# Performance work log

Hardware: AMD Instinct MI355X
Metric: run time of the kernel (lower is better)

The kernel has to match this reference:

```python
import jax, jax.numpy as jnp
import numpy as np

N, F, E, FE, H, OUT = 20000, 128, 320000, 16, 128, 128
NTYPES = 2  # types = (0, 1)
NPAIRS = NTYPES * NTYPES


def setup_inputs() -> dict:
    key = jax.random.key(0)
    ks = jax.random.split(key, 12)
    edge_in_dim = 2 * F + FE
    node_in_dim = F + H
    s = lambda *shape: 1.0 / np.sqrt(shape[-2])
    return {
        "x": jax.random.normal(ks[0], (N, 1, F), dtype=jnp.float32),
        "edge_index": jax.random.randint(ks[1], (2, E), 0, N, dtype=jnp.int64),
        "edge_attr": jax.random.normal(ks[2], (E, FE), dtype=jnp.float32),
        "node_type": jax.random.randint(ks[3], (N,), 0, NTYPES, dtype=jnp.int64),
        # edge MLP params, stacked over the 4 (t1,t2) type pairs
        "ew1": jax.random.normal(ks[4], (NPAIRS, edge_in_dim, H), dtype=jnp.float32) * (1.0 / np.sqrt(edge_in_dim)),
        "eb1": jnp.zeros((NPAIRS, H), dtype=jnp.float32),
        "ew2": jax.random.normal(ks[5], (NPAIRS, H, H), dtype=jnp.float32) * (1.0 / np.sqrt(H)),
        "eb2": jnp.zeros((NPAIRS, H), dtype=jnp.float32),
        # node MLP params, stacked over the 2 node types
        "nw1": jax.random.normal(ks[6], (NTYPES, node_in_dim, H), dtype=jnp.float32) * (1.0 / np.sqrt(node_in_dim)),
        "nb1": jnp.zeros((NTYPES, H), dtype=jnp.float32),
        "nw2": jax.random.normal(ks[7], (NTYPES, H, OUT), dtype=jnp.float32) * (1.0 / np.sqrt(H)),
        "nb2": jnp.zeros((NTYPES, OUT), dtype=jnp.float32),
    }


def reference(x, edge_index, edge_attr, node_type, ew1, eb1, ew2, eb2, nw1, nb1, nw2, nb2):
    x0 = x[:, 0]  # [N, F]
    row, col = edge_index[0], edge_index[1]

    # ---- edge model: type-pair-dispatched 2-layer ReLU MLP ----
    edge_in = jnp.concatenate([x0[row], x0[col], edge_attr], axis=-1)  # [E, 2F+FE]
    h1 = jax.nn.relu(jnp.einsum("ei,pih->eph", edge_in, ew1) + eb1)    # [E, P, H]
    h2 = jax.nn.relu(jnp.einsum("eph,phk->epk", h1, ew2) + eb2)        # [E, P, H]
    pair_id = node_type[row] * NTYPES + node_type[col]                  # [E]
    pair_oh = jax.nn.one_hot(pair_id, NPAIRS, dtype=h2.dtype)           # [E, P]
    edge_feat = jnp.einsum("epk,ep->ek", h2, pair_oh)                   # [E, H]

    # ---- aggregation: sum over incoming edges per source (row) node ----
    agg = jax.ops.segment_sum(edge_feat, row, num_segments=N)           # [N, H]

    # ---- node model: type-dispatched 2-layer MLP + residual ----
    node_in = jnp.concatenate([x0, agg], axis=-1)                       # [N, F+H]
    n1 = jax.nn.relu(jnp.einsum("ni,tih->nth", node_in, nw1) + nb1)     # [N, T, H]
    n2 = jnp.einsum("nth,thk->ntk", n1, nw2) + nb2                      # [N, T, OUT]
    type_oh = jax.nn.one_hot(node_type, NTYPES, dtype=n2.dtype)         # [N, T]
    out = jnp.einsum("ntk,nt->nk", n2, type_oh)                         # [N, OUT]
    out = out + x0[:, :OUT]  # residual
    return out[:, None, :]  # [N, 1, OUT]
```

## Files before the change

### kernel.cpp

```cpp
#include <hip/hip_runtime.h>

#define N_NODES 20000
#define N_EDGES 320000
#define NBINS   (4*N_NODES)
#define SCAN_NBLK 313
#define PRECONV_NBLK 11216
#define HIST_NBLK 1250

typedef unsigned short u16;
typedef __attribute__((ext_vector_type(8))) short bf16x8;
typedef __attribute__((ext_vector_type(4))) float f32x4;
typedef __attribute__((ext_vector_type(4))) unsigned int u32x4;
typedef __attribute__((ext_vector_type(2))) unsigned int u32x2;

__device__ __forceinline__ float b2f(u16 b){
  unsigned u = ((unsigned)b) << 16; float f; __builtin_memcpy(&f, &u, 4); return f;
}
__device__ __forceinline__ u16 f2b(float f){
  unsigned u; __builtin_memcpy(&u, &f, 4); u += 0x7FFF + ((u >> 16) & 1); return (u16)(u >> 16);
}
__device__ __forceinline__ unsigned cvtpk(float a, float b){
  unsigned r;
  asm("v_cvt_pk_bf16_f32 %0, %1, %2" : "=v"(r) : "v"(a), "v"(b));
  return r;
}

#define NX   (N_NODES*128)
#define NW1T (4*288*128)
#define NW2T (4*128*128)
#define NN1  (2*256*128)
#define NN2  (2*128*128)

__global__ void k_prep(const float* __restrict__ x,
                       const float* __restrict__ ew1, const float* __restrict__ ew2,
                       const float* __restrict__ nw1, const float* __restrict__ nw2,
                       u16* __restrict__ x0b,
                       u16* __restrict__ wt1t, u16* __restrict__ wt2t,
                       u16* __restrict__ nw1t, u16* __restrict__ nw2t,
                       const int* __restrict__ ei, const int* __restrict__ ntp,
                       int* __restrict__ hist, int* __restrict__ hist_nt,
                       u16* __restrict__ srank)
{
  int bid = blockIdx.x;
  if (bid >= PRECONV_NBLK) {
    int t = (bid - PRECONV_NBLK) * 256 + threadIdx.x;
    int lane = threadIdx.x & 63;
    if (t < N_EDGES) {
      int r = ei[t], c = ei[N_EDGES + t];
      int tr = ntp[r], tc = ntp[c];
      int key = (tr * 2 + tc) * N_NODES + r;
      int rk = atomicAdd(&hist[key], 1);
      srank[t] = (u16)rk;
    }
    bool valid = t < N_NODES;
    int ty = valid ? ntp[t] : -1;
    unsigned long long m0 = __ballot(ty == 0);
    unsigned long long m1 = __ballot(ty == 1);
    if (lane == 0) {
      int c0 = __popcll(m0), c1 = __popcll(m1);
      if (c0) atomicAdd(&hist_nt[0], c0);
      if (c1) atomicAdd(&hist_nt[1], c1);
    }
    return;
  }
  int t = bid * 256 + threadIdx.x;
  if (t < NX) { x0b[t] = f2b(x[t]); return; }
  t -= NX;
  if (t < NW1T) {
    int p = t / 36864, r = t % 36864; int k = r >> 7, n = r & 127;
    float v = (k < 272) ? ew1[(p * 272 + k) * 128 + n] : 0.f;
    wt1t[(p * 128 + n) * 288 + k] = f2b(v);
    return;
  }
  t -= NW1T;
  if (t < NW2T) {
    int p = t >> 14, r = t & 16383; int k = r >> 7, n = r & 127;
    wt2t[(p * 128 + n) * 128 + k] = f2b(ew2[(p * 128 + k) * 128 + n]);
    return;
  }
  t -= NW2T;
  if (t < NN1) {
    int ty = t >> 15, r = t & 32767; int k = r >> 7, n = r & 127;
    nw1t[(ty * 128 + n) * 256 + k] = f2b(nw1[(ty * 256 + k) * 128 + n]);
    return;
  }
  t -= NN1;
  if (t < NN2) {
    int ty = t >> 14, r = t & 16383; int k = r >> 7, n = r & 127;
    nw2t[(ty * 128 + n) * 128 + k] = f2b(nw2[(ty * 128 + k) * 128 + n]);
  }
}

__global__ void k_scan1(const int* __restrict__ hist, int* __restrict__ parts)
{
  __shared__ int s[256];
  int i = blockIdx.x * 256 + threadIdx.x;
  s[threadIdx.x] = (i < NBINS) ? hist[i] : 0;
  __syncthreads();
  for (int off = 128; off > 0; off >>= 1) {
    if (threadIdx.x < off) s[threadIdx.x] += s[threadIdx.x + off];
    __syncthreads();
  }
  if (threadIdx.x == 0) parts[blockIdx.x] = s[0];
}

__global__ void k_scan2(int* __restrict__ parts)
{
  __shared__ int s[512];
  int t = threadIdx.x;
  int v = (t < SCAN_NBLK) ? parts[t] : 0;
  s[t] = v; __syncthreads();
  for (int off = 1; off < 512; off <<= 1) {
    int xv = (t >= off) ? s[t - off] : 0;
    __syncthreads();
    s[t] += xv;
    __syncthreads();
  }
  if (t < SCAN_NBLK) parts[t] = s[t] - v;
}

__global__ void k_scan3(const int* __restrict__ hist, const int* __restrict__ parts,
                        int* __restrict__ bstart)
{
  __shared__ int s[256];
  int i = blockIdx.x * 256 + threadIdx.x;
  int v = (i < NBINS) ? hist[i] : 0;
  s[threadIdx.x] = v; __syncthreads();
  for (int off = 1; off < 256; off <<= 1) {
    int xv = (threadIdx.x >= off) ? s[threadIdx.x - off] : 0;
    __syncthreads();
    s[threadIdx.x] += xv;
    __syncthreads();
  }
  int excl = s[threadIdx.x] - v + parts[blockIdx.x];
  if (i < NBINS) bstart[i] = excl;
  if (i == 0) bstart[NBINS] = N_EDGES;
}

__global__ void k_place(const int* __restrict__ ei, const int* __restrict__ ntp,
                        const u16* __restrict__ srank, const int* __restrict__ bstart,
                        int2* __restrict__ sedge,
                        int* __restrict__ cur_nt, const int* __restrict__ hist_nt,
                        int* __restrict__ nidx)
{
  int t = blockIdx.x * 256 + threadIdx.x;
  int lane = threadIdx.x & 63;
  if (t < N_EDGES) {
    int r = ei[t], c = ei[N_EDGES + t];
    int tr = ntp[r], tc = ntp[c];
    int key = (tr * 2 + tc) * N_NODES + r;
    int pos = bstart[key] + (int)srank[t];
    int2 v; v.x = r | (c << 15); v.y = t;
    sedge[pos] = v;
  }
  bool valid = t < N_NODES;
  int ty = valid ? ntp[t] : -1;
  unsigned long long m0 = __ballot(ty == 0);
  unsigned long long m1 = __ballot(ty == 1);
  int b0 = 0, b1 = 0;
  if (lane == 0) {
    int c0 = __popcll(m0), c1 = __popcll(m1);
    if (c0) b0 = atomicAdd(&cur_nt[0], c0);
    if (c1) b1 = atomicAdd(&cur_nt[1], c1);
  }
  b0 = __shfl(b0, 0); b1 = __shfl(b1, 0);
  if (valid) {
    unsigned long long lt = (1ull << lane) - 1ull;
    int pos = (ty == 0) ? (b0 + __popcll(m0 & lt))
                        : (hist_nt[0] + b1 + __popcll(m1 & lt));
    nidx[pos] = t;
  }
}

__launch_bounds__(1024, 4)
__global__ void k_edge(const u16* __restrict__ x0b, const float* __restrict__ ea,
                       const u16* __restrict__ wt1t, const u16* __restrict__ wt2t,
                       const float* __restrict__ eb1, const float* __restrict__ eb2,
                       const int* __restrict__ bstart, const int2* __restrict__ sedge,
                       u16* __restrict__ h2s)
{
  __shared__ u16 sW1[128 * 296];
  __shared__ u16 sW2[128 * 136];
  __shared__ u16 slab[16][16][80];
  __shared__ float sEb1[128];
  __shared__ float sEb2[128];

  const int p    = blockIdx.y;
  const int tid  = threadIdx.x;
  const int lane = tid & 63;
  const int wv   = tid >> 6;
  const int llo  = lane & 15;
  const int lhi  = lane >> 4;

  const int base_p = bstart[p * N_NODES];
  const int end_p  = bstart[(p + 1) * N_NODES];

  for (int i = tid; i < 128 * 36; i += 1024) {
    int n = i / 36, c = i % 36;
    *(u32x4*)&sW1[n * 296 + c * 8] = *(const u32x4*)&wt1t[(p * 128 + n) * 288 + c * 8];
  }
  for (int i = tid; i < 128 * 16; i += 1024) {
    int n = i >> 4, c = i & 15;
    *(u32x4*)&sW2[n * 136 + c * 8] = *(const u32x4*)&wt2t[(p * 128 + n) * 128 + c * 8];
  }
  if (tid < 128) sEb1[tid] = eb1[p * 128 + tid];
  else if (tid < 256) sEb2[tid - 128] = eb2[p * 128 + tid - 128];
  __syncthreads();

  for (int g = blockIdx.x * 16 + wv; ; g += gridDim.x * 16) {
    const int es = base_p + g * 32;
    if (es >= end_p) break;

    int pos[2], row[2], col[2], eid[2];
    #pragma unroll
    for (int j = 0; j < 2; ++j) {
      pos[j] = es + j * 16 + llo;
      int pc = pos[j] < end_p ? pos[j] : end_p - 1;
      int2 m = sedge[pc];
      row[j] = m.x & 32767; col[j] = m.x >> 15; eid[j] = m.y;
    }

    bf16x8 xr[2][4], xc[2][4], eaf[2];
    #pragma unroll
    for (int j = 0; j < 2; ++j) {
      #pragma unroll
      for (int ck = 0; ck < 4; ++ck) {
        xr[j][ck] = *(const bf16x8*)&x0b[row[j] * 128 + ck * 32 + lhi * 8];
        xc[j][ck] = *(const bf16x8*)&x0b[col[j] * 128 + ck * 32 + lhi * 8];
      }
      u32x4 pk = (u32x4){0u, 0u, 0u, 0u};
      if (lhi < 2) {
        f32x4 f0 = *(const f32x4*)&ea[eid[j] * 16 + lhi * 8];
        f32x4 f1 = *(const f32x4*)&ea[eid[j] * 16 + lhi * 8 + 4];
        pk[0] = cvtpk(f0[0], f0[1]); pk[1] = cvtpk(f0[2], f0[3]);
        pk[2] = cvtpk(f1[0], f1[1]); pk[3] = cvtpk(f1[2], f1[3]);
      }
      __builtin_memcpy(&eaf[j], &pk, 16);
    }

    f32x4 acc[8][2];
    #pragma unroll
    for (int i = 0; i < 8; ++i) {
      acc[i][0] = (f32x4){0.f, 0.f, 0.f, 0.f};
      acc[i][1] = (f32x4){0.f, 0.f, 0.f, 0.f};
    }

    #pragma unroll
    for (int ck = 0; ck < 4; ++ck) {
      #pragma unroll
      for (int i = 0; i < 8; ++i) {
        bf16x8 wa = *(const bf16x8*)&sW1[(i * 16 + llo) * 296 + ck * 32 + lhi * 8];
        acc[i][0] = __builtin_amdgcn_mfma_f32_16x16x32_bf16(wa, xr[0][ck], acc[i][0], 0, 0, 0);
        acc[i][1] = __builtin_amdgcn_mfma_f32_16x16x32_bf16(wa, xr[1][ck], acc[i][1], 0, 0, 0);
      }
    }
    #pragma unroll
    for (int ck = 0; ck < 4; ++ck) {
      #pragma unroll
      for (int i = 0; i < 8; ++i) {
        bf16x8 wb = *(const bf16x8*)&sW1[(i * 16 + llo) * 296 + 128 + ck * 32 + lhi * 8];
        acc[i][0] = __builtin_amdgcn_mfma_f32_16x16x32_bf16(wb, xc[0][ck], acc[i][0], 0, 0, 0);
        acc[i][1] = __builtin_amdgcn_mfma_f32_16x16x32_bf16(wb, xc[1][ck], acc[i][1], 0, 0, 0);
      }
    }
    #pragma unroll
    for (int i = 0; i < 8; ++i) {
      bf16x8 wce = *(const bf16x8*)&sW1[(i * 16 + llo) * 296 + 256 + lhi * 8];
      acc[i][0] = __builtin_amdgcn_mfma_f32_16x16x32_bf16(wce, eaf[0], acc[i][0], 0, 0, 0);
      acc[i][1] = __builtin_amdgcn_mfma_f32_16x16x32_bf16(wce, eaf[1], acc[i][1], 0, 0, 0);
    }

    bf16x8 h1f[2][4];
    #pragma unroll
    for (int j = 0; j < 2; ++j) {
      #pragma unroll
      for (int ph = 0; ph < 2; ++ph) {
        #pragma unroll
        for (int ii = 0; ii < 4; ++ii) {
          const int i = ph * 4 + ii;
          const f32x4 bb = *(const f32x4*)&sEb1[i * 16 + lhi * 4];
          float v0 = acc[i][j][0] + bb[0]; v0 = v0 > 0.f ? v0 : 0.f;
          float v1 = acc[i][j][1] + bb[1]; v1 = v1 > 0.f ? v1 : 0.f;
          float v2 = acc[i][j][2] + bb[2]; v2 = v2 > 0.f ? v2 : 0.f;
          float v3 = acc[i][j][3] + bb[3]; v3 = v3 > 0.f ? v3 : 0.f;
          u32x2 pk; pk[0] = cvtpk(v0, v1); pk[1] = cvtpk(v2, v3);
          *(u32x2*)&slab[wv][llo][ii * 16 + lhi * 4] = pk;
        }
        #pragma unroll
        for (int cc = 0; cc < 2; ++cc)
          h1f[j][ph * 2 + cc] = *(const bf16x8*)&slab[wv][llo][cc * 32 + lhi * 8];
      }
    }

    f32x4 o[8][2];
    #pragma unroll
    for (int i = 0; i < 8; ++i) {
      o[i][0] = (f32x4){0.f, 0.f, 0.f, 0.f};
      o[i][1] = (f32x4){0.f, 0.f, 0.f, 0.f};
    }
    #pragma unroll
    for (int ck = 0; ck < 4; ++ck) {
      #pragma unroll
      for (int i = 0; i < 8; ++i) {
        bf16x8 w2f = *(const bf16x8*)&sW2[(i * 16 + llo) * 136 + ck * 32 + lhi * 8];
        o[i][0] = __builtin_amdgcn_mfma_f32_16x16x32_bf16(w2f, h1f[0][ck], o[i][0], 0, 0, 0);
        o[i][1] = __builtin_amdgcn_mfma_f32_16x16x32_bf16(w2f, h1f[1][ck], o[i][1], 0, 0, 0);
      }
    }

    #pragma unroll
    for (int i = 0; i < 8; ++i) {
      const f32x4 bb = *(const f32x4*)&sEb2[i * 16 + lhi * 4];
      #pragma unroll
      for (int j = 0; j < 2; ++j) {
        float v0 = o[i][j][0] + bb[0]; v0 = v0 > 0.f ? v0 : 0.f;
        float v1 = o[i][j][1] + bb[1]; v1 = v1 > 0.f ? v1 : 0.f;
        float v2 = o[i][j][2] + bb[2]; v2 = v2 > 0.f ? v2 : 0.f;
        float v3 = o[i][j][3] + bb[3]; v3 = v3 > 0.f ? v3 : 0.f;
        u32x2 pk; pk[0] = cvtpk(v0, v1); pk[1] = cvtpk(v2, v3);
        if (pos[j] < end_p) *(u32x2*)&h2s[pos[j] * 128 + i * 16 + lhi * 4] = pk;
      }
    }
  }
}

__launch_bounds__(512, 1)
__global__ void k_node(const u16* __restrict__ x0b, const float* __restrict__ xf,
                       const u16* __restrict__ h2s,
                       const u16* __restrict__ nw1t, const u16* __restrict__ nw2t,
                       const float* __restrict__ nb1, const float* __restrict__ nb2,
                       const int* __restrict__ bstart,
                       const int* __restrict__ nidx, const int* __restrict__ hist_nt,
                       float* __restrict__ out)
{
  const int ty    = blockIdx.y;
  const int cnt0  = hist_nt[0];
  const int cnt_t = ty ? (N_NODES - cnt0) : cnt0;
  const int base_t = ty ? cnt0 : 0;

  __shared__ u16 sNIN[64 * 264];
  __shared__ u16 sNW1[128 * 264];
  __shared__ u16 sNW2[128 * 136];
  __shared__ float sNb1[128];
  __shared__ float sNb2[128];
  __shared__ int sNid[64];

  const int tid  = threadIdx.x;
  const int lane = tid & 63;
  const int wid  = tid >> 6;
  const int llo  = lane & 15;
  const int lhi  = lane >> 4;

  for (int i = tid; i < 128 * 256; i += 512) {
    int n = i >> 8, k = i & 255;
    sNW1[n * 264 + k] = nw1t[(ty * 128 + n) * 256 + k];
  }
  for (int i = tid; i < 128 * 128; i += 512) {
    int n = i >> 7, k = i & 127;
    sNW2[n * 136 + k] = nw2t[(ty * 128 + n) * 128 + k];
  }
  if (tid < 128) { sNb1[tid] = nb1[ty * 128 + tid]; sNb2[tid] = nb2[ty * 128 + tid]; }
  __syncthreads();

  for (int t0 = blockIdx.x * 64; t0 < cnt_t; t0 += gridDim.x * 64) {
    const int cnt = min(64, cnt_t - t0);
    if (tid < 64) {
      int nid = 0;
      if (tid < cnt) nid = nidx[base_t + t0 + tid];
      sNid[tid] = nid;
    }
    __syncthreads();

    {
      const int m = tid >> 3, qq = tid & 7;
      const int nid = sNid[m];
      const u16* xs = &x0b[nid * 128 + qq * 16];
      u16* dst = &sNIN[m * 264 + qq * 16];
      #pragma unroll
      for (int j = 0; j < 2; ++j) *(u32x4*)(dst + j * 8) = *(const u32x4*)(xs + j * 8);

      float a[16];
      #pragma unroll
      for (int j = 0; j < 16; ++j) a[j] = 0.f;
      #pragma unroll
      for (int pr = 0; pr < 2; ++pr) {
        const int key = (ty * 2 + pr) * N_NODES + nid;
        const int s = bstart[key], e = bstart[key + 1];
        for (int pos = s; pos < e; ++pos) {
          const u16* hp = &h2s[pos * 128 + qq * 16];
          #pragma unroll
          for (int j = 0; j < 2; ++j) {
            u32x4 v = *(const u32x4*)(hp + j * 8);
            #pragma unroll
            for (int w = 0; w < 4; ++w) {
              unsigned uu = v[w];
              a[j * 8 + w * 2 + 0] += b2f((u16)(uu & 0xFFFFu));
              a[j * 8 + w * 2 + 1] += b2f((u16)(uu >> 16));
            }
          }
        }
      }
      u16* ad = &sNIN[m * 264 + 128 + qq * 16];
      #pragma unroll
      for (int j = 0; j < 8; ++j) {
        unsigned pk = cvtpk(a[2 * j], a[2 * j + 1]);
        *(unsigned*)(ad + 2 * j) = pk;
      }
    }
    __syncthreads();

    f32x4 acc[4];
    #pragma unroll
    for (int i = 0; i < 4; ++i) acc[i] = (f32x4){0.f, 0.f, 0.f, 0.f};

    #pragma unroll
    for (int ck = 0; ck < 8; ++ck) {
      const int kk = ck * 32 + lhi * 8;
      bf16x8 a[4], b;
      #pragma unroll
      for (int i = 0; i < 4; ++i)
        a[i] = *(const bf16x8*)&sNIN[(i * 16 + llo) * 264 + kk];
      b = *(const bf16x8*)&sNW1[(wid * 16 + llo) * 264 + kk];
      #pragma unroll
      for (int i = 0; i < 4; ++i)
        acc[i] = __builtin_amdgcn_mfma_f32_16x16x32_bf16(a[i], b, acc[i], 0, 0, 0);
    }
    __syncthreads();

    u16* sH1 = sNIN;
    #pragma unroll
    for (int i = 0; i < 4; ++i) {
      const int c = wid * 16 + llo;
      const float bias = sNb1[c];
      #pragma unroll
      for (int r = 0; r < 4; ++r) {
        const int m = i * 16 + lhi * 4 + r;
        float v = acc[i][r] + bias;
        v = v > 0.f ? v : 0.f;
        sH1[m * 136 + c] = f2b(v);
      }
    }
    __syncthreads();

    #pragma unroll
    for (int i = 0; i < 4; ++i) acc[i] = (f32x4){0.f, 0.f, 0.f, 0.f};

    #pragma unroll
    for (int ck = 0; ck < 4; ++ck) {
      const int kk = ck * 32 + lhi * 8;
      bf16x8 a[4], b;
      #pragma unroll
      for (int i = 0; i < 4; ++i)
        a[i] = *(const bf16x8*)&sH1[(i * 16 + llo) * 136 + kk];
      b = *(const bf16x8*)&sNW2[(wid * 16 + llo) * 136 + kk];
      #pragma unroll
      for (int i = 0; i < 4; ++i)
        acc[i] = __builtin_amdgcn_mfma_f32_16x16x32_bf16(a[i], b, acc[i], 0, 0, 0);
    }

    #pragma unroll
    for (int i = 0; i < 4; ++i) {
      const int c = wid * 16 + llo;
      const float bias = sNb2[c];
      #pragma unroll
      for (int r = 0; r < 4; ++r) {
        const int m = i * 16 + lhi * 4 + r;
        if (m < cnt) {
          const int nid = sNid[m];
          out[nid * 128 + c] = acc[i][r] + bias + xf[nid * 128 + c];
        }
      }
    }
    __syncthreads();
  }
}

extern "C" void kernel_launch(void* const* d_in, const int* in_sizes, int n_in,
                              void* d_out, int out_size, void* d_ws, size_t ws_size,
                              hipStream_t stream)
{
  const float* x   = (const float*)d_in[0];
  const int*   ei  = (const int*)d_in[1];
  const float* ea  = (const float*)d_in[2];
  const int*   ntp = (const int*)d_in[3];
  const float* ew1 = (const float*)d_in[4];
  const float* eb1 = (const float*)d_in[5];
  const float* ew2 = (const float*)d_in[6];
  const float* eb2 = (const float*)d_in[7];
  const float* nw1 = (const float*)d_in[8];
  const float* nb1 = (const float*)d_in[9];
  const float* nw2 = (const float*)d_in[10];
  const float* nb2 = (const float*)d_in[11];

  char* ws = (char*)d_ws;
  int*  hist    = (int*)(ws + 0);
  int*  hist_nt = (int*)(ws + 320000);
  int*  cur_nt  = (int*)(ws + 320008);
  int*  parts   = (int*)(ws + 320256);
  int*  bstart  = (int*)(ws + 321792);
  u16*  srank   = (u16*)(ws + 641824);
  int2* sedge   = (int2*)(ws + 1281824);
  int*  nidx    = (int*)(ws + 3841824);
  u16*  x0b     = (u16*)(ws + 3921824);
  u16*  wt1t    = (u16*)(ws + 9041824);
  u16*  wt2t    = (u16*)(ws + 9336736);
  u16*  nw1t    = (u16*)(ws + 9467808);
  u16*  nw2t    = (u16*)(ws + 9598880);
  u16*  h2s     = (u16*)(ws + 9664416);

  hipMemsetAsync(ws, 0, 320016, stream);
  k_prep<<<PRECONV_NBLK + HIST_NBLK, 256, 0, stream>>>(
      x, ew1, ew2, nw1, nw2, x0b, wt1t, wt2t, nw1t, nw2t,
      ei, ntp, hist, hist_nt, srank);
  k_scan1<<<SCAN_NBLK, 256, 0, stream>>>(hist, parts);
  k_scan2<<<1, 512, 0, stream>>>(parts);
  k_scan3<<<SCAN_NBLK, 256, 0, stream>>>(hist, parts, bstart);
  k_place<<<1250, 256, 0, stream>>>(ei, ntp, srank, bstart, sedge, cur_nt, hist_nt, nidx);
  k_edge<<<dim3(64, 4), 1024, 0, stream>>>(x0b, ea, wt1t, wt2t, eb1, eb2, bstart, sedge, h2s);
  k_node<<<dim3(160, 2), 512, 0, stream>>>(x0b, x, h2s, nw1t, nw2t, nb1, nb2, bstart, nidx, hist_nt, (float*)d_out);
}
```

Before: 184.0 us.

## Double-buffer edge tile gathers in k_edge with software pipelining

Restructures the edge MLP kernel so each wave prefetches the next 32-edge tile's gathered node features and edge attributes into registers while it computes the current tile, ping-ponging between two tile buffers. The block shrinks from 1024 to 512 threads and the per-wave slab widens so the h1 transpose is done in one pass. The goal is to hide gather latency behind MFMA work. In exchange, register pressure roughly doubles for the input fragments and there are fewer waves per block, which may reduce occupancy.

```diff
diff --git a/kernel.cpp b/kernel.cpp
--- a/kernel.cpp
+++ b/kernel.cpp
@@ -172,7 +172,125 @@
   }
 }
 
-__launch_bounds__(1024, 4)
+struct ETile {
+  int pos[2];
+  bf16x8 xr[2][4], xc[2][4], eaf[2];
+};
+
+__device__ __forceinline__ void load_tile(ETile& T, int es, int end_p,
+    const int2* __restrict__ sedge, const u16* __restrict__ x0b,
+    const float* __restrict__ ea, int llo, int lhi)
+{
+  #pragma unroll
+  for (int j = 0; j < 2; ++j) {
+    int pos = es + j * 16 + llo;
+    T.pos[j] = pos;
+    int pc = pos < end_p ? pos : end_p - 1;
+    int2 m = sedge[pc];
+    int row = m.x & 32767, col = m.x >> 15, eid = m.y;
+    #pragma unroll
+    for (int ck = 0; ck < 4; ++ck) {
+      T.xr[j][ck] = *(const bf16x8*)&x0b[row * 128 + ck * 32 + lhi * 8];
+      T.xc[j][ck] = *(const bf16x8*)&x0b[col * 128 + ck * 32 + lhi * 8];
+    }
+    u32x4 pk = (u32x4){0u, 0u, 0u, 0u};
+    if (lhi < 2) {
+      f32x4 f0 = *(const f32x4*)&ea[eid * 16 + lhi * 8];
+      f32x4 f1 = *(const f32x4*)&ea[eid * 16 + lhi * 8 + 4];
+      pk[0] = cvtpk(f0[0], f0[1]); pk[1] = cvtpk(f0[2], f0[3]);
+      pk[2] = cvtpk(f1[0], f1[1]); pk[3] = cvtpk(f1[2], f1[3]);
+    }
+    __builtin_memcpy(&T.eaf[j], &pk, 16);
+  }
+}
+
+__device__ __forceinline__ void compute_tile(const ETile& T,
+    const u16* sW1, const u16* sW2, u16* myslab,
+    const float* sEb1, const float* sEb2,
+    u16* __restrict__ h2s, int end_p, int llo, int lhi)
+{
+  f32x4 acc[8][2];
+  #pragma unroll
+  for (int i = 0; i < 8; ++i) {
+    acc[i][0] = (f32x4){0.f, 0.f, 0.f, 0.f};
+    acc[i][1] = (f32x4){0.f, 0.f, 0.f, 0.f};
+  }
+
+  #pragma unroll
+  for (int ck = 0; ck < 4; ++ck) {
+    #pragma unroll
+    for (int i = 0; i < 8; ++i) {
+      bf16x8 wa = *(const bf16x8*)&sW1[(i * 16 + llo) * 296 + ck * 32 + lhi * 8];
+      acc[i][0] = __builtin_amdgcn_mfma_f32_16x16x32_bf16(wa, T.xr[0][ck], acc[i][0], 0, 0, 0);
+      acc[i][1] = __builtin_amdgcn_mfma_f32_16x16x32_bf16(wa, T.xr[1][ck], acc[i][1], 0, 0, 0);
+    }
+  }
+  #pragma unroll
+  for (int ck = 0; ck < 4; ++ck) {
+    #pragma unroll
+    for (int i = 0; i < 8; ++i) {
+      bf16x8 wb = *(const bf16x8*)&sW1[(i * 16 + llo) * 296 + 128 + ck * 32 + lhi * 8];
+      acc[i][0] = __builtin_amdgcn_mfma_f32_16x16x32_bf16(wb, T.xc[0][ck], acc[i][0], 0, 0, 0);
+      acc[i][1] = __builtin_amdgcn_mfma_f32_16x16x32_bf16(wb, T.xc[1][ck], acc[i][1], 0, 0, 0);
+    }
+  }
+  #pragma unroll
+  for (int i = 0; i < 8; ++i) {
+    bf16x8 wce = *(const bf16x8*)&sW1[(i * 16 + llo) * 296 + 256 + lhi * 8];
+    acc[i][0] = __builtin_amdgcn_mfma_f32_16x16x32_bf16(wce, T.eaf[0], acc[i][0], 0, 0, 0);
+    acc[i][1] = __builtin_amdgcn_mfma_f32_16x16x32_bf16(wce, T.eaf[1], acc[i][1], 0, 0, 0);
+  }
+
+  bf16x8 h1f[2][4];
+  #pragma unroll
+  for (int j = 0; j < 2; ++j) {
+    #pragma unroll
+    for (int i = 0; i < 8; ++i) {
+      const f32x4 bb = *(const f32x4*)&sEb1[i * 16 + lhi * 4];
+      float v0 = acc[i][j][0] + bb[0]; v0 = v0 > 0.f ? v0 : 0.f;
+      float v1 = acc[i][j][1] + bb[1]; v1 = v1 > 0.f ? v1 : 0.f;
+      float v2 = acc[i][j][2] + bb[2]; v2 = v2 > 0.f ? v2 : 0.f;
+      float v3 = acc[i][j][3] + bb[3]; v3 = v3 > 0.f ? v3 : 0.f;
+      u32x2 pk; pk[0] = cvtpk(v0, v1); pk[1] = cvtpk(v2, v3);
+      *(u32x2*)&myslab[llo * 136 + i * 16 + lhi * 4] = pk;
+    }
+    #pragma unroll
+    for (int ck = 0; ck < 4; ++ck)
+      h1f[j][ck] = *(const bf16x8*)&myslab[llo * 136 + ck * 32 + lhi * 8];
+  }
+
+  f32x4 o[8][2];
+  #pragma unroll
+  for (int i = 0; i < 8; ++i) {
+    o[i][0] = (f32x4){0.f, 0.f, 0.f, 0.f};
+    o[i][1] = (f32x4){0.f, 0.f, 0.f, 0.f};
+  }
+  #pragma unroll
+  for (int ck = 0; ck < 4; ++ck) {
+    #pragma unroll
+    for (int i = 0; i < 8; ++i) {
+      bf16x8 w2f = *(const bf16x8*)&sW2[(i * 16 + llo) * 136 + ck * 32 + lhi * 8];
+      o[i][0] = __builtin_amdgcn_mfma_f32_16x16x32_bf16(w2f, h1f[0][ck], o[i][0], 0, 0, 0);
+      o[i][1] = __builtin_amdgcn_mfma_f32_16x16x32_bf16(w2f, h1f[1][ck], o[i][1], 0, 0, 0);
+    }
+  }
+
+  #pragma unroll
+  for (int i = 0; i < 8; ++i) {
+    const f32x4 bb = *(const f32x4*)&sEb2[i * 16 + lhi * 4];
+    #pragma unroll
+    for (int j = 0; j < 2; ++j) {
+      float v0 = o[i][j][0] + bb[0]; v0 = v0 > 0.f ? v0 : 0.f;
+      float v1 = o[i][j][1] + bb[1]; v1 = v1 > 0.f ? v1 : 0.f;
+      float v2 = o[i][j][2] + bb[2]; v2 = v2 > 0.f ? v2 : 0.f;
+      float v3 = o[i][j][3] + bb[3]; v3 = v3 > 0.f ? v3 : 0.f;
+      u32x2 pk; pk[0] = cvtpk(v0, v1); pk[1] = cvtpk(v2, v3);
+      if (T.pos[j] < end_p) *(u32x2*)&h2s[T.pos[j] * 128 + i * 16 + lhi * 4] = pk;
+    }
+  }
+}
+
+__launch_bounds__(512, 2)
 __global__ void k_edge(const u16* __restrict__ x0b, const float* __restrict__ ea,
                        const u16* __restrict__ wt1t, const u16* __restrict__ wt2t,
                        const float* __restrict__ eb1, const float* __restrict__ eb2,
@@ -181,7 +299,7 @@
 {
   __shared__ u16 sW1[128 * 296];
   __shared__ u16 sW2[128 * 136];
-  __shared__ u16 slab[16][16][80];
+  __shared__ u16 slab[8][16][136];
   __shared__ float sEb1[128];
   __shared__ float sEb2[128];
 
@@ -195,11 +313,11 @@
   const int base_p = bstart[p * N_NODES];
   const int end_p  = bstart[(p + 1) * N_NODES];
 
-  for (int i = tid; i < 128 * 36; i += 1024) {
+  for (int i = tid; i < 128 * 36; i += 512) {
     int n = i / 36, c = i % 36;
     *(u32x4*)&sW1[n * 296 + c * 8] = *(const u32x4*)&wt1t[(p * 128 + n) * 288 + c * 8];
   }
-  for (int i = tid; i < 128 * 16; i += 1024) {
+  for (int i = tid; i < 128 * 16; i += 512) {
     int n = i >> 4, c = i & 15;
     *(u32x4*)&sW2[n * 136 + c * 8] = *(const u32x4*)&wt2t[(p * 128 + n) * 128 + c * 8];
   }
@@ -207,120 +325,25 @@
   else if (tid < 256) sEb2[tid - 128] = eb2[p * 128 + tid - 128];
   __syncthreads();
 
-  for (int g = blockIdx.x * 16 + wv; ; g += gridDim.x * 16) {
-    const int es = base_p + g * 32;
-    if (es >= end_p) break;
-
-    int pos[2], row[2], col[2], eid[2];
-    #pragma unroll
-    for (int j = 0; j < 2; ++j) {
-      pos[j] = es + j * 16 + llo;
-      int pc = pos[j] < end_p ? pos[j] : end_p - 1;
-      int2 m = sedge[pc];
-      row[j] = m.x & 32767; col[j] = m.x >> 15; eid[j] = m.y;
-    }
-
-    bf16x8 xr[2][4], xc[2][4], eaf[2];
-    #pragma unroll
-    for (int j = 0; j < 2; ++j) {
-      #pragma unroll
-      for (int ck = 0; ck < 4; ++ck) {
-        xr[j][ck] = *(const bf16x8*)&x0b[row[j] * 128 + ck * 32 + lhi * 8];
-        xc[j][ck] = *(const bf16x8*)&x0b[col[j] * 128 + ck * 32 + lhi * 8];
-      }
-      u32x4 pk = (u32x4){0u, 0u, 0u, 0u};
-      if (lhi < 2) {
-        f32x4 f0 = *(const f32x4*)&ea[eid[j] * 16 + lhi * 8];
-        f32x4 f1 = *(const f32x4*)&ea[eid[j] * 16 + lhi * 8 + 4];
-        pk[0] = cvtpk(f0[0], f0[1]); pk[1] = cvtpk(f0[2], f0[3]);
-        pk[2] = cvtpk(f1[0], f1[1]); pk[3] = cvtpk(f1[2], f1[3]);
-      }
-      __builtin_memcpy(&eaf[j], &pk, 16);
-    }
-
-    f32x4 acc[8][2];
-    #pragma unroll
-    for (int i = 0; i < 8; ++i) {
-      acc[i][0] = (f32x4){0.f, 0.f, 0.f, 0.f};
-      acc[i][1] = (f32x4){0.f, 0.f, 0.f, 0.f};
-    }
-
-    #pragma unroll
-    for (int ck = 0; ck < 4; ++ck) {
-      #pragma unroll
-      for (int i = 0; i < 8; ++i) {
-        bf16x8 wa = *(const bf16x8*)&sW1[(i * 16 + llo) * 296 + ck * 32 + lhi * 8];
-        acc[i][0] = __builtin_amdgcn_mfma_f32_16x16x32_bf16(wa, xr[0][ck], acc[i][0], 0, 0, 0);
-        acc[i][1] = __builtin_amdgcn_mfma_f32_16x16x32_bf16(wa, xr[1][ck], acc[i][1], 0, 0, 0);
-      }
-    }
-    #pragma unroll
-    for (int ck = 0; ck < 4; ++ck) {
-      #pragma unroll
-      for (int i = 0; i < 8; ++i) {
-        bf16x8 wb = *(const bf16x8*)&sW1[(i * 16 + llo) * 296 + 128 + ck * 32 + lhi * 8];
-        acc[i][0] = __builtin_amdgcn_mfma_f32_16x16x32_bf16(wb, xc[0][ck], acc[i][0], 0, 0, 0);
-        acc[i][1] = __builtin_amdgcn_mfma_f32_16x16x32_bf16(wb, xc[1][ck], acc[i][1], 0, 0, 0);
-      }
-    }
-    #pragma unroll
-    for (int i = 0; i < 8; ++i) {
-      bf16x8 wce = *(const bf16x8*)&sW1[(i * 16 + llo) * 296 + 256 + lhi * 8];
-      acc[i][0] = __builtin_amdgcn_mfma_f32_16x16x32_bf16(wce, eaf[0], acc[i][0], 0, 0, 0);
-      acc[i][1] = __builtin_amdgcn_mfma_f32_16x16x32_bf16(wce, eaf[1], acc[i][1], 0, 0, 0);
-    }
-
-    bf16x8 h1f[2][4];
-    #pragma unroll
-    for (int j = 0; j < 2; ++j) {
-      #pragma unroll
-      for (int ph = 0; ph < 2; ++ph) {
-        #pragma unroll
-        for (int ii = 0; ii < 4; ++ii) {
-          const int i = ph * 4 + ii;
-          const f32x4 bb = *(const f32x4*)&sEb1[i * 16 + lhi * 4];
-          float v0 = acc[i][j][0] + bb[0]; v0 = v0 > 0.f ? v0 : 0.f;
-          float v1 = acc[i][j][1] + bb[1]; v1 = v1 > 0.f ? v1 : 0.f;
-          float v2 = acc[i][j][2] + bb[2]; v2 = v2 > 0.f ? v2 : 0.f;
-          float v3 = acc[i][j][3] + bb[3]; v3 = v3 > 0.f ? v3 : 0.f;
-          u32x2 pk; pk[0] = cvtpk(v0, v1); pk[1] = cvtpk(v2, v3);
-          *(u32x2*)&slab[wv][llo][ii * 16 + lhi * 4] = pk;
-        }
-        #pragma unroll
-        for (int cc = 0; cc < 2; ++cc)
-          h1f[j][ph * 2 + cc] = *(const bf16x8*)&slab[wv][llo][cc * 32 + lhi * 8];
-      }
-    }
-
-    f32x4 o[8][2];
-    #pragma unroll
-    for (int i = 0; i < 8; ++i) {
-      o[i][0] = (f32x4){0.f, 0.f, 0.f, 0.f};
-      o[i][1] = (f32x4){0.f, 0.f, 0.f, 0.f};
-    }
-    #pragma unroll
-    for (int ck = 0; ck < 4; ++ck) {
-      #pragma unroll
-      for (int i = 0; i < 8; ++i) {
-        bf16x8 w2f = *(const bf16x8*)&sW2[(i * 16 + llo) * 136 + ck * 32 + lhi * 8];
-        o[i][0] = __builtin_amdgcn_mfma_f32_16x16x32_bf16(w2f, h1f[0][ck], o[i][0], 0, 0, 0);
-        o[i][1] = __builtin_amdgcn_mfma_f32_16x16x32_bf16(w2f, h1f[1][ck], o[i][1], 0, 0, 0);
-      }
-    }
-
-    #pragma unroll
-    for (int i = 0; i < 8; ++i) {
-      const f32x4 bb = *(const f32x4*)&sEb2[i * 16 + lhi * 4];
-      #pragma unroll
-      for (int j = 0; j < 2; ++j) {
-        float v0 = o[i][j][0] + bb[0]; v0 = v0 > 0.f ? v0 : 0.f;
-        float v1 = o[i][j][1] + bb[1]; v1 = v1 > 0.f ? v1 : 0.f;
-        float v2 = o[i][j][2] + bb[2]; v2 = v2 > 0.f ? v2 : 0.f;
-        float v3 = o[i][j][3] + bb[3]; v3 = v3 > 0.f ? v3 : 0.f;
-        u32x2 pk; pk[0] = cvtpk(v0, v1); pk[1] = cvtpk(v2, v3);
-        if (pos[j] < end_p) *(u32x2*)&h2s[pos[j] * 128 + i * 16 + lhi * 4] = pk;
-      }
-    }
+  u16* myslab = &slab[wv][0][0];
+  const int stride = gridDim.x * 256;
+  int es = base_p + blockIdx.x * 256 + wv * 32;
+  if (es >= end_p) return;
+
+  ETile TA, TB;
+  load_tile(TA, es, end_p, sedge, x0b, ea, llo, lhi);
+  while (true) {
+    int esn = es + stride;
+    bool hn = esn < end_p;
+    if (hn) load_tile(TB, esn, end_p, sedge, x0b, ea, llo, lhi);
+    compute_tile(TA, sW1, sW2, myslab, sEb1, sEb2, h2s, end_p, llo, lhi);
+    if (!hn) break;
+    es = esn;
+    esn = es + stride; hn = esn < end_p;
+    if (hn) load_tile(TA, esn, end_p, sedge, x0b, ea, llo, lhi);
+    compute_tile(TB, sW1, sW2, myslab, sEb1, sEb2, h2s, end_p, llo, lhi);
+    if (!hn) break;
+    es = esn;
   }
 }
 
@@ -516,6 +539,6 @@
   k_scan2<<<1, 512, 0, stream>>>(parts);
   k_scan3<<<SCAN_NBLK, 256, 0, stream>>>(hist, parts, bstart);
   k_place<<<1250, 256, 0, stream>>>(ei, ntp, srank, bstart, sedge, cur_nt, hist_nt, nidx);
-  k_edge<<<dim3(64, 4), 1024, 0, stream>>>(x0b, ea, wt1t, wt2t, eb1, eb2, bstart, sedge, h2s);
+  k_edge<<<dim3(64, 4), 512, 0, stream>>>(x0b, ea, wt1t, wt2t, eb1, eb2, bstart, sedge, h2s);
   k_node<<<dim3(160, 2), 512, 0, stream>>>(x0b, x, h2s, nw1t, nw2t, nb1, nb2, bstart, nidx, hist_nt, (float*)d_out);
 }
```

Result: slower. 590.3 us (+220.9%).

## Halve edge-kernel block size, prefetch next tile's edge metadata, widen h1 slab

Applied to the files above, without the earlier changes.

The edge MLP kernel now runs 512-thread blocks (8 waves) instead of 1024, with per-block contiguous 256-edge tiles strided across the grid. It prefetches the sorted edge metadata for the next tile while the current tile's gathers and MFMAs run, hiding that dependent load latency. The h1 staging slab is widened to a full 128-column row per lane group, so the bias/ReLU/pack and reload happen in one pass instead of two halves. Halving the threads per block with the same grid halves the waves in flight and puts more edges on each wave, which may reduce latency hiding; the larger slab also raises shared memory use.

```diff
diff --git a/kernel.cpp b/kernel.cpp
--- a/kernel.cpp
+++ b/kernel.cpp
@@ -172,7 +172,7 @@
   }
 }
 
-__launch_bounds__(1024, 4)
+__launch_bounds__(512, 2)
 __global__ void k_edge(const u16* __restrict__ x0b, const float* __restrict__ ea,
                        const u16* __restrict__ wt1t, const u16* __restrict__ wt2t,
                        const float* __restrict__ eb1, const float* __restrict__ eb2,
@@ -181,7 +181,7 @@
 {
   __shared__ u16 sW1[128 * 296];
   __shared__ u16 sW2[128 * 136];
-  __shared__ u16 slab[16][16][80];
+  __shared__ u16 slab[8][16][136];
   __shared__ float sEb1[128];
   __shared__ float sEb2[128];
 
@@ -195,11 +195,11 @@
   const int base_p = bstart[p * N_NODES];
   const int end_p  = bstart[(p + 1) * N_NODES];
 
-  for (int i = tid; i < 128 * 36; i += 1024) {
+  for (int i = tid; i < 128 * 36; i += 512) {
     int n = i / 36, c = i % 36;
     *(u32x4*)&sW1[n * 296 + c * 8] = *(const u32x4*)&wt1t[(p * 128 + n) * 288 + c * 8];
   }
-  for (int i = tid; i < 128 * 16; i += 1024) {
+  for (int i = tid; i < 128 * 16; i += 512) {
     int n = i >> 4, c = i & 15;
     *(u32x4*)&sW2[n * 136 + c * 8] = *(const u32x4*)&wt2t[(p * 128 + n) * 128 + c * 8];
   }
@@ -207,35 +207,59 @@
   else if (tid < 256) sEb2[tid - 128] = eb2[p * 128 + tid - 128];
   __syncthreads();
 
-  for (int g = blockIdx.x * 16 + wv; ; g += gridDim.x * 16) {
-    const int es = base_p + g * 32;
-    if (es >= end_p) break;
-
-    int pos[2], row[2], col[2], eid[2];
-    #pragma unroll
-    for (int j = 0; j < 2; ++j) {
-      pos[j] = es + j * 16 + llo;
-      int pc = pos[j] < end_p ? pos[j] : end_p - 1;
-      int2 m = sedge[pc];
-      row[j] = m.x & 32767; col[j] = m.x >> 15; eid[j] = m.y;
-    }
+  u16* myslab = &slab[wv][0][0];
+  const int stride = gridDim.x * 256;
+  const int ts0 = base_p + blockIdx.x * 256;
+
+  int2 mN0 = {0, 0}, mN1 = {0, 0};
+  if (ts0 < end_p) {
+    const int e0 = ts0 + wv * 32;
+    int q0 = e0 + llo;       q0 = q0 < end_p ? q0 : end_p - 1;
+    int q1 = e0 + 16 + llo;  q1 = q1 < end_p ? q1 : end_p - 1;
+    mN0 = sedge[q0];
+    mN1 = sedge[q1];
+  }
+
+  for (int ts = ts0; ts < end_p; ts += stride) {
+    const int pos0 = ts + wv * 32 + llo;
+    const int pos1 = pos0 + 16;
+    const int row0 = mN0.x & 32767, col0 = mN0.x >> 15, eid0 = mN0.y;
+    const int row1 = mN1.x & 32767, col1 = mN1.x >> 15, eid1 = mN1.y;
 
     bf16x8 xr[2][4], xc[2][4], eaf[2];
     #pragma unroll
-    for (int j = 0; j < 2; ++j) {
-      #pragma unroll
-      for (int ck = 0; ck < 4; ++ck) {
-        xr[j][ck] = *(const bf16x8*)&x0b[row[j] * 128 + ck * 32 + lhi * 8];
-        xc[j][ck] = *(const bf16x8*)&x0b[col[j] * 128 + ck * 32 + lhi * 8];
-      }
-      u32x4 pk = (u32x4){0u, 0u, 0u, 0u};
+    for (int ck = 0; ck < 4; ++ck) {
+      xr[0][ck] = *(const bf16x8*)&x0b[row0 * 128 + ck * 32 + lhi * 8];
+      xc[0][ck] = *(const bf16x8*)&x0b[col0 * 128 + ck * 32 + lhi * 8];
+      xr[1][ck] = *(const bf16x8*)&x0b[row1 * 128 + ck * 32 + lhi * 8];
+      xc[1][ck] = *(const bf16x8*)&x0b[col1 * 128 + ck * 32 + lhi * 8];
+    }
+    {
+      u32x4 pk0 = (u32x4){0u, 0u, 0u, 0u};
+      u32x4 pk1 = (u32x4){0u, 0u, 0u, 0u};
       if (lhi < 2) {
-        f32x4 f0 = *(const f32x4*)&ea[eid[j] * 16 + lhi * 8];
-        f32x4 f1 = *(const f32x4*)&ea[eid[j] * 16 + lhi * 8 + 4];
-        pk[0] = cvtpk(f0[0], f0[1]); pk[1] = cvtpk(f0[2], f0[3]);
-        pk[2] = cvtpk(f1[0], f1[1]); pk[3] = cvtpk(f1[2], f1[3]);
-      }
-      __builtin_memcpy(&eaf[j], &pk, 16);
+        f32x4 f0 = *(const f32x4*)&ea[eid0 * 16 + lhi * 8];
+        f32x4 f1 = *(const f32x4*)&ea[eid0 * 16 + lhi * 8 + 4];
+        pk0[0] = cvtpk(f0[0], f0[1]); pk0[1] = cvtpk(f0[2], f0[3]);
+        pk0[2] = cvtpk(f1[0], f1[1]); pk0[3] = cvtpk(f1[2], f1[3]);
+        f32x4 g0 = *(const f32x4*)&ea[eid1 * 16 + lhi * 8];
+        f32x4 g1 = *(const f32x4*)&ea[eid1 * 16 + lhi * 8 + 4];
+        pk1[0] = cvtpk(g0[0], g0[1]); pk1[1] = cvtpk(g0[2], g0[3]);
+        pk1[2] = cvtpk(g1[0], g1[1]); pk1[3] = cvtpk(g1[2], g1[3]);
+      }
+      __builtin_memcpy(&eaf[0], &pk0, 16);
+      __builtin_memcpy(&eaf[1], &pk1, 16);
+    }
+
+    {
+      const int tn = ts + stride;
+      if (tn < end_p) {
+        const int e0n = tn + wv * 32;
+        int q0 = e0n + llo;       q0 = q0 < end_p ? q0 : end_p - 1;
+        int q1 = e0n + 16 + llo;  q1 = q1 < end_p ? q1 : end_p - 1;
+        mN0 = sedge[q0];
+        mN1 = sedge[q1];
+      }
     }
 
     f32x4 acc[8][2];
@@ -274,22 +298,18 @@
     #pragma unroll
     for (int j = 0; j < 2; ++j) {
       #pragma unroll
-      for (int ph = 0; ph < 2; ++ph) {
-        #pragma unroll
-        for (int ii = 0; ii < 4; ++ii) {
-          const int i = ph * 4 + ii;
-          const f32x4 bb = *(const f32x4*)&sEb1[i * 16 + lhi * 4];
-          float v0 = acc[i][j][0] + bb[0]; v0 = v0 > 0.f ? v0 : 0.f;
-          float v1 = acc[i][j][1] + bb[1]; v1 = v1 > 0.f ? v1 : 0.f;
-          float v2 = acc[i][j][2] + bb[2]; v2 = v2 > 0.f ? v2 : 0.f;
-          float v3 = acc[i][j][3] + bb[3]; v3 = v3 > 0.f ? v3 : 0.f;
-          u32x2 pk; pk[0] = cvtpk(v0, v1); pk[1] = cvtpk(v2, v3);
-          *(u32x2*)&slab[wv][llo][ii * 16 + lhi * 4] = pk;
-        }
-        #pragma unroll
-        for (int cc = 0; cc < 2; ++cc)
-          h1f[j][ph * 2 + cc] = *(const bf16x8*)&slab[wv][llo][cc * 32 + lhi * 8];
-      }
+      for (int i = 0; i < 8; ++i) {
+        const f32x4 bb = *(const f32x4*)&sEb1[i * 16 + lhi * 4];
+        float v0 = acc[i][j][0] + bb[0]; v0 = v0 > 0.f ? v0 : 0.f;
+        float v1 = acc[i][j][1] + bb[1]; v1 = v1 > 0.f ? v1 : 0.f;
+        float v2 = acc[i][j][2] + bb[2]; v2 = v2 > 0.f ? v2 : 0.f;
+        float v3 = acc[i][j][3] + bb[3]; v3 = v3 > 0.f ? v3 : 0.f;
+        u32x2 pk; pk[0] = cvtpk(v0, v1); pk[1] = cvtpk(v2, v3);
+        *(u32x2*)&myslab[llo * 136 + i * 16 + lhi * 4] = pk;
+      }
+      #pragma unroll
+      for (int ck = 0; ck < 4; ++ck)
+        h1f[j][ck] = *(const bf16x8*)&myslab[llo * 136 + ck * 32 + lhi * 8];
     }
 
     f32x4 o[8][2];
@@ -311,14 +331,21 @@
     #pragma unroll
     for (int i = 0; i < 8; ++i) {
       const f32x4 bb = *(const f32x4*)&sEb2[i * 16 + lhi * 4];
-      #pragma unroll
-      for (int j = 0; j < 2; ++j) {
-        float v0 = o[i][j][0] + bb[0]; v0 = v0 > 0.f ? v0 : 0.f;
-        float v1 = o[i][j][1] + bb[1]; v1 = v1 > 0.f ? v1 : 0.f;
-        float v2 = o[i][j][2] + bb[2]; v2 = v2 > 0.f ? v2 : 0.f;
-        float v3 = o[i][j][3] + bb[3]; v3 = v3 > 0.f ? v3 : 0.f;
+      {
+        float v0 = o[i][0][0] + bb[0]; v0 = v0 > 0.f ? v0 : 0.f;
+        float v1 = o[i][0][1] + bb[1]; v1 = v1 > 0.f ? v1 : 0.f;
+        float v2 = o[i][0][2] + bb[2]; v2 = v2 > 0.f ? v2 : 0.f;
+        float v3 = o[i][0][3] + bb[3]; v3 = v3 > 0.f ? v3 : 0.f;
         u32x2 pk; pk[0] = cvtpk(v0, v1); pk[1] = cvtpk(v2, v3);
-        if (pos[j] < end_p) *(u32x2*)&h2s[pos[j] * 128 + i * 16 + lhi * 4] = pk;
+        if (pos0 < end_p) *(u32x2*)&h2s[pos0 * 128 + i * 16 + lhi * 4] = pk;
+      }
+      {
+        float v0 = o[i][1][0] + bb[0]; v0 = v0 > 0.f ? v0 : 0.f;
+        float v1 = o[i][1][1] + bb[1]; v1 = v1 > 0.f ? v1 : 0.f;
+        float v2 = o[i][1][2] + bb[2]; v2 = v2 > 0.f ? v2 : 0.f;
+        float v3 = o[i][1][3] + bb[3]; v3 = v3 > 0.f ? v3 : 0.f;
+        u32x2 pk; pk[0] = cvtpk(v0, v1); pk[1] = cvtpk(v2, v3);
+        if (pos1 < end_p) *(u32x2*)&h2s[pos1 * 128 + i * 16 + lhi * 4] = pk;
       }
     }
   }
@@ -516,6 +543,6 @@
   k_scan2<<<1, 512, 0, stream>>>(parts);
   k_scan3<<<SCAN_NBLK, 256, 0, stream>>>(hist, parts, bstart);
   k_place<<<1250, 256, 0, stream>>>(ei, ntp, srank, bstart, sedge, cur_nt, hist_nt, nidx);
-  k_edge<<<dim3(64, 4), 1024, 0, stream>>>(x0b, ea, wt1t, wt2t, eb1, eb2, bstart, sedge, h2s);
+  k_edge<<<dim3(64, 4), 512, 0, stream>>>(x0b, ea, wt1t, wt2t, eb1, eb2, bstart, sedge, h2s);
   k_node<<<dim3(160, 2), 512, 0, stream>>>(x0b, x, h2s, nw1t, nw2t, nb1, nb2, bstart, nidx, hist_nt, (float*)d_out);
 }
```

Result: faster. 166.5 us (-9.5%).
